# Performance work log

Measured on AMD Instinct MI355X. Metric: run time of the kernel, lower is better.

Reference implementation:

```python
import jax, jax.numpy as jnp
import numpy as np

N, E, G, T = 4096, 16384, 128, 100
DIMS = [(5, 64), (64, 128), (128, 256)]
EPS = 1e-5


def setup_inputs() -> dict:
    key = jax.random.key(0)
    ks = iter(jax.random.split(key, 64))
    d = {}
    d["x"] = jax.random.normal(next(ks), (N, 5), jnp.float32)
    d["edge_index"] = jax.random.randint(next(ks), (2, E), 0, N, jnp.int64)
    d["edge_attr"] = jax.random.uniform(next(ks), (E, 3), jnp.float32)
    d["batch_seg"] = jnp.sort(jax.random.randint(next(ks), (N,), 0, G, jnp.int64))
    for l, (cin, cout) in enumerate(DIMS, start=1):
        d[f"l{l}_W1"] = jax.random.normal(next(ks), (3, 32), jnp.float32) * 0.3
        d[f"l{l}_b1"] = jnp.zeros((32,), jnp.float32)
        d[f"l{l}_W2"] = jax.random.normal(next(ks), (32, cin * cout), jnp.float32) * 0.05
        d[f"l{l}_b2"] = jnp.zeros((cin * cout,), jnp.float32)
        d[f"l{l}_root"] = jax.random.normal(next(ks), (cin, cout), jnp.float32) * 0.1
        d[f"l{l}_bias"] = jnp.zeros((cout,), jnp.float32)
        d[f"bn{l}_g"] = jnp.ones((cout,), jnp.float32)
        d[f"bn{l}_b"] = jnp.zeros((cout,), jnp.float32)
        d[f"bn{l}_m"] = jax.random.normal(next(ks), (cout,), jnp.float32) * 0.01
        d[f"bn{l}_v"] = jax.random.uniform(next(ks), (cout,), jnp.float32, 0.5, 1.5)
    d["mlp_W"] = jax.random.normal(next(ks), (256, T), jnp.float32) * 0.06
    d["mlp_b"] = jnp.zeros((T,), jnp.float32)
    return d


def _nnconv(h, src, dst, edge_attr, W1, b1, W2, b2, root, bias, cin, cout):
    # edge MLP -> per-edge weight matrix [E, cin, cout]
    ew = (jax.nn.relu(edge_attr @ W1 + b1) @ W2 + b2).reshape(-1, cin, cout)
    msg = jnp.einsum('ei,eio->eo', h[src], ew)  # gather + per-edge matmul
    ssum = jax.ops.segment_sum(msg, dst, num_segments=N)
    cnt = jax.ops.segment_sum(jnp.ones((msg.shape[0],), msg.dtype), dst, num_segments=N)
    agg = ssum / jnp.maximum(cnt, 1.0)[:, None]  # scatter-mean
    return h @ root + agg + bias


def _bn(h, g, b, m, v):
    return g * (h - m) * jax.lax.rsqrt(v + EPS) + b


def reference(x, edge_index, edge_attr, batch_seg,
              l1_W1, l1_b1, l1_W2, l1_b2, l1_root, l1_bias, bn1_g, bn1_b, bn1_m, bn1_v,
              l2_W1, l2_b1, l2_W2, l2_b2, l2_root, l2_bias, bn2_g, bn2_b, bn2_m, bn2_v,
              l3_W1, l3_b1, l3_W2, l3_b2, l3_root, l3_bias, bn3_g, bn3_b, bn3_m, bn3_v,
              mlp_W, mlp_b):
    src, dst = edge_index[0], edge_index[1]
    h = _nnconv(x, src, dst, edge_attr, l1_W1, l1_b1, l1_W2, l1_b2, l1_root, l1_bias, 5, 64)
    h = jax.nn.relu(_bn(h, bn1_g, bn1_b, bn1_m, bn1_v))
    h = _nnconv(h, src, dst, edge_attr, l2_W1, l2_b1, l2_W2, l2_b2, l2_root, l2_bias, 64, 128)
    h = jax.nn.relu(_bn(h, bn2_g, bn2_b, bn2_m, bn2_v))
    h = _nnconv(h, src, dst, edge_attr, l3_W1, l3_b1, l3_W2, l3_b2, l3_root, l3_bias, 128, 256)
    h = jax.nn.relu(_bn(h, bn3_g, bn3_b, bn3_m, bn3_v))
    # global mean pool over graphs
    psum = jax.ops.segment_sum(h, batch_seg, num_segments=G)
    pcnt = jax.ops.segment_sum(jnp.ones((N,), h.dtype), batch_seg, num_segments=G)
    pooled = psum / jnp.maximum(pcnt, 1.0)[:, None]
    out = pooled @ mlp_W + mlp_b
    return jnp.where(out > 0, out, 0.1 * out)  # LeakyReLU(0.1)
```

## Files before the change

kernel.cpp:

```cpp
#include <hip/hip_runtime.h>
#include <cstdint>
#include <cstddef>

#define BN_EPS 1e-5f

typedef short bf16x8 __attribute__((ext_vector_type(8)));
typedef float f32x4  __attribute__((ext_vector_type(4)));
typedef unsigned short u16x8 __attribute__((ext_vector_type(8)));

__device__ __forceinline__ uint16_t f2bf_rte(float f) {
  uint32_t u = __float_as_uint(f);
  uint32_t r = u + 0x7fffu + ((u >> 16) & 1u);
  return (uint16_t)(r >> 16);
}
__device__ __forceinline__ float bf2f(uint16_t h) {
  return __uint_as_float(((uint32_t)h) << 16);
}
__device__ __forceinline__ void split_bf(float v, uint16_t& hi, uint16_t& lo) {
  hi = f2bf_rte(v);
  lo = f2bf_rte(v - bf2f(hi));
}

__device__ __forceinline__ void glds16(const uint16_t* g, uint16_t* l) {
  __builtin_amdgcn_global_load_lds(
      (const __attribute__((address_space(1))) uint32_t*)(const void*)g,
      (__attribute__((address_space(3))) uint32_t*)(void*)l, 16, 0, 0);
}

__global__ __launch_bounds__(1024) void csr_all_k(const int* __restrict__ dst,
                                                  int* __restrict__ offsets,
                                                  int* __restrict__ csr,
                                                  int N, int E) {
  __shared__ int cntS[4096];
  __shared__ int part[1024];
  const int t = threadIdx.x;
  for (int i = t; i < N; i += 1024) cntS[i] = 0;
  __syncthreads();
  for (int e = t; e < E; e += 1024) atomicAdd(&cntS[dst[e]], 1);
  __syncthreads();
  int a0 = cntS[4*t+0], a1 = cntS[4*t+1], a2 = cntS[4*t+2], a3 = cntS[4*t+3];
  part[t] = a0 + a1 + a2 + a3;
  __syncthreads();
  for (int off = 1; off < 1024; off <<= 1) {
    int v = (t >= off) ? part[t - off] : 0;
    __syncthreads();
    part[t] += v;
    __syncthreads();
  }
  int excl = (t == 0) ? 0 : part[t-1];
  int o0 = excl, o1 = o0 + a0, o2 = o1 + a1, o3 = o2 + a2;
  cntS[4*t+0] = o0; cntS[4*t+1] = o1; cntS[4*t+2] = o2; cntS[4*t+3] = o3;
  offsets[4*t+0] = o0; offsets[4*t+1] = o1; offsets[4*t+2] = o2; offsets[4*t+3] = o3;
  if (t == 0) offsets[N] = E;
  __syncthreads();
  for (int e = t; e < E; e += 1024) {
    int d = dst[e];
    int pos = atomicAdd(&cntS[d], 1);
    csr[pos] = e;
  }
}

__device__ __forceinline__ void w_elem(const float* __restrict__ W2, const float* __restrict__ b2,
                                       const float* __restrict__ root,
                                       uint16_t* __restrict__ Hi, uint16_t* __restrict__ Lo,
                                       int cin, int cout, int Kpad, int li) {
  int o  = li / Kpad;
  int ki = li - o * Kpad;
  float v = 0.f;
  if (ki < 34 * cin) {
    int k = ki / cin;
    int i = ki - k * cin;
    if (k < 32)       v = W2[(size_t)k * cin * cout + (size_t)i * cout + o];
    else if (k == 32) v = b2[(size_t)i * cout + o];
    else              v = root[(size_t)i * cout + o];
  }
  uint16_t hi, lo;
  split_bf(v, hi, lo);
  Hi[li] = hi;
  Lo[li] = lo;
}

__global__ void build_W3_k(const float* __restrict__ W2a, const float* __restrict__ b2a,
                           const float* __restrict__ roota, uint16_t* __restrict__ Hia,
                           uint16_t* __restrict__ Loa,
                           const float* __restrict__ W2b, const float* __restrict__ b2b,
                           const float* __restrict__ rootb, uint16_t* __restrict__ Hib,
                           uint16_t* __restrict__ Lob,
                           const float* __restrict__ W2c, const float* __restrict__ b2c,
                           const float* __restrict__ rootc, uint16_t* __restrict__ Hic,
                           uint16_t* __restrict__ Loc,
                           int e0, int e1, int e2) {
  int idx = blockIdx.x * blockDim.x + threadIdx.x;
  if (idx < e0)      w_elem(W2a, b2a, roota, Hia, Loa, 5,   64,  192,  idx);
  else if (idx < e1) w_elem(W2b, b2b, rootb, Hib, Lob, 64,  128, 2176, idx - e0);
  else if (idx < e2) w_elem(W2c, b2c, rootc, Hic, Loc, 128, 256, 4352, idx - e1);
}

template<int CIN>
__global__ __launch_bounds__(256) void build_S_vec_k(const float* __restrict__ h,
                                                     const float* __restrict__ ea,
                                                     const float* __restrict__ W1,
                                                     const float* __restrict__ b1,
                                                     const int* __restrict__ src,
                                                     const int* __restrict__ csr,
                                                     const int* __restrict__ offsets,
                                                     uint16_t* __restrict__ Shi,
                                                     uint16_t* __restrict__ Slo,
                                                     int Kpad) {
  constexpr int CH = 8;
  constexpr int K1 = 33 * CIN;
  constexpr int NCH = K1 / 8;
  constexpr int NP = (NCH + 255) / 256;
  __shared__ float hs[CH][CIN];
  __shared__ float zs[CH][33];
  __shared__ int   es[CH];
  const int n = blockIdx.x;
  const int tid = threadIdx.x;
  const int base = offsets[n];
  const int deg  = offsets[n+1] - base;
  const float scale = 1.f / fmaxf((float)deg, 1.f);
  float acc[NP][8];
#pragma unroll
  for (int p = 0; p < NP; p++)
#pragma unroll
    for (int j = 0; j < 8; j++) acc[p][j] = 0.f;

  for (int c0 = 0; c0 < deg; c0 += CH) {
    const int cc = min(CH, deg - c0);
    if (tid < cc) es[tid] = csr[base + c0 + tid];
    __syncthreads();
    for (int idx = tid; idx < cc * CIN; idx += 256) {
      int slot = idx / CIN, i = idx - slot * CIN;
      hs[slot][i] = h[(size_t)src[es[slot]] * CIN + i];
    }
    for (int idx = tid; idx < cc * 33; idx += 256) {
      int slot = idx / 33, k = idx - slot * 33;
      float v;
      if (k == 32) v = 1.f;
      else {
        int e = es[slot];
        v = fmaxf(ea[e*3+0] * W1[k] + ea[e*3+1] * W1[32 + k] + ea[e*3+2] * W1[64 + k] + b1[k], 0.f);
      }
      zs[slot][k] = v;
    }
    __syncthreads();
#pragma unroll
    for (int p = 0; p < NP; p++) {
      int ch = p * 256 + tid;
      if (ch < NCH) {
        int ki0 = ch * 8;
        int k  = ki0 / CIN;
        int i0 = ki0 & (CIN - 1);
        for (int c = 0; c < cc; c++) {
          float zv = zs[c][k];
          float4 h0 = *(const float4*)&hs[c][i0];
          float4 h1 = *(const float4*)&hs[c][i0 + 4];
          acc[p][0] += zv * h0.x; acc[p][1] += zv * h0.y;
          acc[p][2] += zv * h0.z; acc[p][3] += zv * h0.w;
          acc[p][4] += zv * h1.x; acc[p][5] += zv * h1.y;
          acc[p][6] += zv * h1.z; acc[p][7] += zv * h1.w;
        }
      }
    }
    __syncthreads();
  }
  const size_t rowb = (size_t)n * Kpad;
#pragma unroll
  for (int p = 0; p < NP; p++) {
    int ch = p * 256 + tid;
    if (ch < NCH) {
      u16x8 hv, lv;
#pragma unroll
      for (int j = 0; j < 8; j++) {
        uint16_t hi, lo;
        split_bf(acc[p][j] * scale, hi, lo);
        hv[j] = hi; lv[j] = lo;
      }
      *(u16x8*)(Shi + rowb + ch * 8) = hv;
      *(u16x8*)(Slo + rowb + ch * 8) = lv;
    }
  }
  for (int c = tid; c < CIN / 8; c += 256) {
    int i0 = c * 8;
    float4 a = *(const float4*)&h[(size_t)n * CIN + i0];
    float4 b = *(const float4*)&h[(size_t)n * CIN + i0 + 4];
    float vals[8] = {a.x, a.y, a.z, a.w, b.x, b.y, b.z, b.w};
    u16x8 hv, lv;
#pragma unroll
    for (int j = 0; j < 8; j++) {
      uint16_t hi, lo;
      split_bf(vals[j], hi, lo);
      hv[j] = hi; lv[j] = lo;
    }
    *(u16x8*)(Shi + rowb + K1 + i0) = hv;
    *(u16x8*)(Slo + rowb + K1 + i0) = lv;
  }
  for (int ki = 34 * CIN + tid; ki < Kpad; ki += 256) {
    Shi[rowb + ki] = 0;
    Slo[rowb + ki] = 0;
  }
}

__global__ __launch_bounds__(256) void build_S5_k(const float* __restrict__ h,
                                                  const float* __restrict__ ea,
                                                  const float* __restrict__ W1,
                                                  const float* __restrict__ b1,
                                                  const int* __restrict__ src,
                                                  const int* __restrict__ csr,
                                                  const int* __restrict__ offsets,
                                                  uint16_t* __restrict__ Shi,
                                                  uint16_t* __restrict__ Slo,
                                                  int Kpad) {
  constexpr int CIN = 5, CH = 8;
  constexpr int K1 = 33 * CIN;
  constexpr int KT = 34 * CIN;
  __shared__ float hs[CH][CIN];
  __shared__ float zs[CH][33];
  __shared__ int   es[CH];
  const int n = blockIdx.x;
  const int tid = threadIdx.x;
  const int base = offsets[n];
  const int deg  = offsets[n+1] - base;
  const float scale = 1.f / fmaxf((float)deg, 1.f);
  float acc = 0.f;

  for (int c0 = 0; c0 < deg; c0 += CH) {
    const int cc = min(CH, deg - c0);
    if (tid < cc) es[tid] = csr[base + c0 + tid];
    __syncthreads();
    for (int idx = tid; idx < cc * CIN; idx += 256) {
      int slot = idx / CIN, i = idx - slot * CIN;
      hs[slot][i] = h[(size_t)src[es[slot]] * CIN + i];
    }
    for (int idx = tid; idx < cc * 33; idx += 256) {
      int slot = idx / 33, k = idx - slot * 33;
      float v;
      if (k == 32) v = 1.f;
      else {
        int e = es[slot];
        v = fmaxf(ea[e*3+0] * W1[k] + ea[e*3+1] * W1[32 + k] + ea[e*3+2] * W1[64 + k] + b1[k], 0.f);
      }
      zs[slot][k] = v;
    }
    __syncthreads();
    if (tid < K1) {
      int k = tid / CIN, i = tid - (tid / CIN) * CIN;
      float a = acc;
      for (int c = 0; c < cc; c++) a += zs[c][k] * hs[c][i];
      acc = a;
    }
    __syncthreads();
  }
  const size_t rowb = (size_t)n * Kpad;
  if (tid < K1) {
    uint16_t hi, lo;
    split_bf(acc * scale, hi, lo);
    Shi[rowb + tid] = hi;
    Slo[rowb + tid] = lo;
  }
  if (tid < CIN) {
    uint16_t hi, lo;
    split_bf(h[(size_t)n * CIN + tid], hi, lo);
    Shi[rowb + K1 + tid] = hi;
    Slo[rowb + K1 + tid] = lo;
  }
  for (int ki = KT + tid; ki < Kpad; ki += 256) {
    Shi[rowb + ki] = 0;
    Slo[rowb + ki] = 0;
  }
}

template<int BN, int KS>
__global__ __launch_bounds__(256, 1) void mfma_gemm2_k(const uint16_t* __restrict__ Ahi,
                                                       const uint16_t* __restrict__ Alo,
                                                       const uint16_t* __restrict__ Bhi,
                                                       const uint16_t* __restrict__ Blo,
                                                       float* __restrict__ Cpart,
                                                       int Kpad, int Ncol, int M,
                                                       int totalIters) {
  constexpr int BM = 128;
  constexpr int FN = BN / 32;
  constexpr int SLOTS = KS / 8;
  constexpr int RPC = 2048 / KS;
  constexpr int NCA = BM / RPC;
  constexpr int NCB = BN / RPC;
  constexpr int OAH = 0;
  constexpr int OAL = BM * KS;
  constexpr int OBH = 2 * BM * KS;
  constexpr int OBL = 2 * BM * KS + BN * KS;
  constexpr int BUFSZ = (2 * BM + 2 * BN) * KS;
  __shared__ uint16_t smem[2 * BUFSZ] __attribute__((aligned(16)));

  const int z  = blockIdx.x;
  const int m0 = blockIdx.y * BM;
  const int n0 = blockIdx.z * BN;
  const int SK = gridDim.x;
  const int itBeg = (int)((long long)totalIters * z / SK);
  const int itEnd = (int)((long long)totalIters * (z + 1) / SK);
  const int nsteps = itEnd - itBeg;

  const int tid  = threadIdx.x;
  const int lane = tid & 63;
  const int wave = tid >> 6;
  const int wm = wave & 1, wn = wave >> 1;
  const int q  = lane >> 4;
  const int mr = lane & 15;

  const int srow  = tid / SLOTS;
  const int sslot = tid & (SLOTS - 1);
  const int sx    = (KS == 64) ? (srow & 7) : ((srow >> 1) & 3);
  const int swz   = (sslot ^ sx) * 8;
  size_t aoff[NCA], boff[NCB];
#pragma unroll
  for (int c = 0; c < NCA; c++)
    aoff[c] = (size_t)(m0 + c * RPC + srow) * Kpad + swz + (size_t)itBeg * KS;
#pragma unroll
  for (int c = 0; c < NCB; c++)
    boff[c] = (size_t)(n0 + c * RPC + srow) * Kpad + swz + (size_t)itBeg * KS;
  const int wlds = wave << 9;

  f32x4 acc[4][FN];
#pragma unroll
  for (int a = 0; a < 4; a++)
#pragma unroll
    for (int b = 0; b < FN; b++) acc[a][b] = (f32x4)0.f;

  auto stage = [&](int buf, int t) {
    uint16_t* base = smem + buf * BUFSZ;
    const size_t ka = (size_t)t * KS;
#pragma unroll
    for (int c = 0; c < NCA; c++) {
      glds16(Ahi + aoff[c] + ka, base + OAH + c * 2048 + wlds);
      glds16(Alo + aoff[c] + ka, base + OAL + c * 2048 + wlds);
    }
#pragma unroll
    for (int c = 0; c < NCB; c++) {
      glds16(Bhi + boff[c] + ka, base + OBH + c * 2048 + wlds);
      glds16(Blo + boff[c] + ka, base + OBL + c * 2048 + wlds);
    }
  };

  const int xr = (KS == 64) ? (mr & 7) : ((mr >> 1) & 3);

  if (nsteps > 0) stage(0, 0);
  for (int t = 0; t < nsteps; t++) {
    __syncthreads();
    if (t + 1 < nsteps) stage((t & 1) ^ 1, t + 1);
    const uint16_t* B_ = smem + (t & 1) * BUFSZ;
#pragma unroll
    for (int ks = 0; ks < KS / 32; ks++) {
      const int e0 = (ks * 32 + q * 8) ^ (xr << 3);
      bf16x8 ah[4], al[4], bh[FN], bl[FN];
#pragma unroll
      for (int f = 0; f < 4; f++) {
        const int row = wm * 64 + f * 16 + mr;
        ah[f] = *(const bf16x8*)&B_[OAH + row * KS + e0];
        al[f] = *(const bf16x8*)&B_[OAL + row * KS + e0];
      }
#pragma unroll
      for (int f = 0; f < FN; f++) {
        const int row = wn * (BN / 2) + f * 16 + mr;
        bh[f] = *(const bf16x8*)&B_[OBH + row * KS + e0];
        bl[f] = *(const bf16x8*)&B_[OBL + row * KS + e0];
      }
#pragma unroll
      for (int fm = 0; fm < 4; fm++)
#pragma unroll
        for (int fn = 0; fn < FN; fn++) {
          acc[fm][fn] = __builtin_amdgcn_mfma_f32_16x16x32_bf16(ah[fm], bh[fn], acc[fm][fn], 0, 0, 0);
          acc[fm][fn] = __builtin_amdgcn_mfma_f32_16x16x32_bf16(ah[fm], bl[fn], acc[fm][fn], 0, 0, 0);
          acc[fm][fn] = __builtin_amdgcn_mfma_f32_16x16x32_bf16(al[fm], bh[fn], acc[fm][fn], 0, 0, 0);
        }
    }
  }

  float* Cz = Cpart + (size_t)z * M * Ncol;
#pragma unroll
  for (int fm = 0; fm < 4; fm++) {
#pragma unroll
    for (int reg = 0; reg < 4; reg++) {
      const int row = m0 + wm * 64 + fm * 16 + q * 4 + reg;
#pragma unroll
      for (int fn = 0; fn < FN; fn++) {
        const int col = n0 + wn * (BN / 2) + fn * 16 + mr;
        Cz[(size_t)row * Ncol + col] = acc[fm][fn][reg];
      }
    }
  }
}

__global__ void epilogue_k(const float* __restrict__ Cpart, int SK, size_t plane4,
                           int Ncol,
                           const float* __restrict__ bias, const float* __restrict__ bg,
                           const float* __restrict__ bb, const float* __restrict__ bnm,
                           const float* __restrict__ bnv,
                           float* __restrict__ C, int total4) {
  int i = blockIdx.x * blockDim.x + threadIdx.x;
  if (i >= total4) return;
  float4 v = {0.f, 0.f, 0.f, 0.f};
  for (int z = 0; z < SK; z++) {
    float4 p = *((const float4*)Cpart + (size_t)z * plane4 + i);
    v.x += p.x; v.y += p.y; v.z += p.z; v.w += p.w;
  }
  int col0 = (i * 4) % Ncol;
  float o[4] = {v.x, v.y, v.z, v.w};
#pragma unroll
  for (int j = 0; j < 4; j++) {
    int c = col0 + j;
    float s = bg[c] * rsqrtf(bnv[c] + BN_EPS);
    float val = (o[j] + bias[c] - bnm[c]) * s + bb[c];
    o[j] = fmaxf(val, 0.f);
  }
  float4 r = {o[0], o[1], o[2], o[3]};
  *((float4*)C + i) = r;
}

__global__ __launch_bounds__(256) void pool_final_k(const float* __restrict__ h,
                                                    const int* __restrict__ seg,
                                                    const float* __restrict__ W,
                                                    const float* __restrict__ b,
                                                    float* __restrict__ out,
                                                    int N, int T) {
  __shared__ float pooled[256];
  const int g = blockIdx.x, tid = threadIdx.x;
  int lo = 0, hi = N;
  while (lo < hi) { int mid = (lo + hi) >> 1; if (seg[mid] < g) lo = mid + 1; else hi = mid; }
  int lo2 = lo, hi2 = N;
  while (lo2 < hi2) { int mid = (lo2 + hi2) >> 1; if (seg[mid] < g + 1) lo2 = mid + 1; else hi2 = mid; }
  const int cnt = lo2 - lo;
  const float inv = 1.f / fmaxf((float)cnt, 1.f);
  float s = 0.f;
  for (int n = lo; n < lo2; n++) s += h[(size_t)n * 256 + tid];
  pooled[tid] = s * inv;
  __syncthreads();
  if (tid < T) {
    float acc = b[tid];
    for (int o = 0; o < 256; o++) acc += pooled[o] * W[(size_t)o * T + tid];
    out[(size_t)g * T + tid] = (acc > 0.f) ? acc : 0.1f * acc;
  }
}

extern "C" void kernel_launch(void* const* d_in, const int* in_sizes, int n_in,
                              void* d_out, int out_size, void* d_ws, size_t ws_size,
                              hipStream_t stream) {
  const float* x   = (const float*)d_in[0];
  const int*   ei  = (const int*)d_in[1];
  const float* ea  = (const float*)d_in[2];
  const int*   seg = (const int*)d_in[3];

  const int N = in_sizes[0] / 5;
  const int E = in_sizes[2] / 3;
  const int T = in_sizes[35];
  const int G = out_size / T;
  const int* src = ei;
  const int* dst = ei + E;

  const float *W1[3], *b1[3], *W2[3], *b2[3], *root[3], *bias[3];
  const float *bng[3], *bnb[3], *bnm[3], *bnv[3];
  for (int l = 0; l < 3; l++) {
    int base = 4 + l * 10;
    W1[l]   = (const float*)d_in[base + 0];
    b1[l]   = (const float*)d_in[base + 1];
    W2[l]   = (const float*)d_in[base + 2];
    b2[l]   = (const float*)d_in[base + 3];
    root[l] = (const float*)d_in[base + 4];
    bias[l] = (const float*)d_in[base + 5];
    bng[l]  = (const float*)d_in[base + 6];
    bnb[l]  = (const float*)d_in[base + 7];
    bnm[l]  = (const float*)d_in[base + 8];
    bnv[l]  = (const float*)d_in[base + 9];
  }
  const float* mlpW = (const float*)d_in[34];
  const float* mlpb = (const float*)d_in[35];

  char* p = (char*)d_ws;
  auto carve = [&](size_t bytes) -> char* {
    char* r = p;
    p += (bytes + 255) & ~(size_t)255;
    return r;
  };
  const int KPADMAX = 4352;
  const int cins[3]   = {5, 64, 128};
  const int couts[3]  = {64, 128, 256};
  const int kpads[3]  = {192, 2176, 4352};
  const int sks[3]    = {3, 8, 8};
  const int ksteps[3] = {64, 64, 32};

  int*      offsets = (int*)carve((size_t)(N + 1) * 4);
  int*      csr     = (int*)carve((size_t)E * 4);
  uint16_t* WhiL[3]; uint16_t* WloL[3];
  for (int l = 0; l < 3; l++) {
    WhiL[l] = (uint16_t*)carve((size_t)couts[l] * kpads[l] * 2);
    WloL[l] = (uint16_t*)carve((size_t)couts[l] * kpads[l] * 2);
  }
  uint16_t* Shi     = (uint16_t*)carve((size_t)N * KPADMAX * 2);
  uint16_t* Slo     = (uint16_t*)carve((size_t)N * KPADMAX * 2);
  float*    Cpart   = (float*)carve((size_t)8 * N * 256 * 4);
  float*    hA      = (float*)carve((size_t)N * 256 * 4);
  float*    hB      = (float*)carve((size_t)N * 128 * 4);

  csr_all_k<<<1, 1024, 0, stream>>>(dst, offsets, csr, N, E);

  {
    int t0 = couts[0] * kpads[0];
    int t1 = couts[1] * kpads[1];
    int t2 = couts[2] * kpads[2];
    int e0 = t0, e1 = t0 + t1, e2 = t0 + t1 + t2;
    build_W3_k<<<(e2 + 255) / 256, 256, 0, stream>>>(
        W2[0], b2[0], root[0], WhiL[0], WloL[0],
        W2[1], b2[1], root[1], WhiL[1], WloL[1],
        W2[2], b2[2], root[2], WhiL[2], WloL[2],
        e0, e1, e2);
  }

  const float* hin = x;
  float* houts[3] = {hA, hB, hA};

  for (int l = 0; l < 3; l++) {
    int cin = cins[l], cout = couts[l], Kpad = kpads[l], SK = sks[l];
    int iters = Kpad / ksteps[l];
    if (cin == 5)
      build_S5_k<<<N, 256, 0, stream>>>(hin, ea, W1[l], b1[l], src, csr, offsets, Shi, Slo, Kpad);
    else if (cin == 64)
      build_S_vec_k<64><<<N, 256, 0, stream>>>(hin, ea, W1[l], b1[l], src, csr, offsets, Shi, Slo, Kpad);
    else
      build_S_vec_k<128><<<N, 256, 0, stream>>>(hin, ea, W1[l], b1[l], src, csr, offsets, Shi, Slo, Kpad);

    if (cout == 256) {
      dim3 grid(SK, N / 128, 1);
      mfma_gemm2_k<256, 32><<<grid, 256, 0, stream>>>(Shi, Slo, WhiL[l], WloL[l], Cpart,
                                                      Kpad, cout, N, iters);
    } else if (cout == 128) {
      dim3 grid(SK, N / 128, 1);
      mfma_gemm2_k<128, 64><<<grid, 256, 0, stream>>>(Shi, Slo, WhiL[l], WloL[l], Cpart,
                                                      Kpad, cout, N, iters);
    } else {
      dim3 grid(SK, N / 128, 1);
      mfma_gemm2_k<64, 64><<<grid, 256, 0, stream>>>(Shi, Slo, WhiL[l], WloL[l], Cpart,
                                                     Kpad, cout, N, iters);
    }

    int total4 = N * cout / 4;
    epilogue_k<<<(total4 + 255) / 256, 256, 0, stream>>>(Cpart, SK, (size_t)N * cout / 4, cout,
                                                         bias[l], bng[l], bnb[l], bnm[l], bnv[l],
                                                         houts[l], total4);
    hin = houts[l];
  }

  pool_final_k<<<G, 256, 0, stream>>>(hA, seg, mlpW, mlpb, (float*)d_out, N, T);
}
```

Measured before the change: 283.5 us.

## Raise GEMM occupancy with single-buffered wide tile and uniform split-K of sixteen

Replaces the split-K MFMA GEMM with a variant that allows two blocks per CU and uses a K step of 32 for every layer. For the cout=256 layer it drops LDS double buffering and reorders the inner loop to load B fragments per column, which cuts LDS and register use so more blocks fit per CU. Split-K rises to 16 for all layers, giving more parallelism but larger partial buffers for the epilogue to reduce. The single-buffered path gives up overlap of global-to-LDS loads with MFMA work within a block and adds a second barrier per step.

```diff
diff --git a/kernel.cpp b/kernel.cpp
--- a/kernel.cpp
+++ b/kernel.cpp
@@ -270,8 +270,8 @@
   }
 }
 
-template<int BN, int KS>
-__global__ __launch_bounds__(256, 1) void mfma_gemm2_k(const uint16_t* __restrict__ Ahi,
+template<int BN, int KS, bool DBUF>
+__global__ __launch_bounds__(256, 2) void mfma_gemm3_k(const uint16_t* __restrict__ Ahi,
                                                        const uint16_t* __restrict__ Alo,
                                                        const uint16_t* __restrict__ Bhi,
                                                        const uint16_t* __restrict__ Blo,
@@ -289,7 +289,8 @@
   constexpr int OBH = 2 * BM * KS;
   constexpr int OBL = 2 * BM * KS + BN * KS;
   constexpr int BUFSZ = (2 * BM + 2 * BN) * KS;
-  __shared__ uint16_t smem[2 * BUFSZ] __attribute__((aligned(16)));
+  constexpr int NB = DBUF ? 2 : 1;
+  __shared__ uint16_t smem[NB * BUFSZ] __attribute__((aligned(16)));
 
   const int z  = blockIdx.x;
   const int m0 = blockIdx.y * BM;
@@ -342,35 +343,67 @@
 
   const int xr = (KS == 64) ? (mr & 7) : ((mr >> 1) & 3);
 
-  if (nsteps > 0) stage(0, 0);
-  for (int t = 0; t < nsteps; t++) {
-    __syncthreads();
-    if (t + 1 < nsteps) stage((t & 1) ^ 1, t + 1);
-    const uint16_t* B_ = smem + (t & 1) * BUFSZ;
-#pragma unroll
-    for (int ks = 0; ks < KS / 32; ks++) {
-      const int e0 = (ks * 32 + q * 8) ^ (xr << 3);
-      bf16x8 ah[4], al[4], bh[FN], bl[FN];
-#pragma unroll
-      for (int f = 0; f < 4; f++) {
-        const int row = wm * 64 + f * 16 + mr;
-        ah[f] = *(const bf16x8*)&B_[OAH + row * KS + e0];
-        al[f] = *(const bf16x8*)&B_[OAL + row * KS + e0];
-      }
-#pragma unroll
-      for (int f = 0; f < FN; f++) {
-        const int row = wn * (BN / 2) + f * 16 + mr;
-        bh[f] = *(const bf16x8*)&B_[OBH + row * KS + e0];
-        bl[f] = *(const bf16x8*)&B_[OBL + row * KS + e0];
-      }
-#pragma unroll
-      for (int fm = 0; fm < 4; fm++)
+  if (DBUF) {
+    if (nsteps > 0) stage(0, 0);
+    for (int t = 0; t < nsteps; t++) {
+      __syncthreads();
+      if (t + 1 < nsteps) stage((t & 1) ^ 1, t + 1);
+      const uint16_t* B_ = smem + (t & 1) * BUFSZ;
+#pragma unroll
+      for (int ks = 0; ks < KS / 32; ks++) {
+        const int e0 = (ks * 32 + q * 8) ^ (xr << 3);
+        bf16x8 ah[4], al[4], bh[FN], bl[FN];
+#pragma unroll
+        for (int f = 0; f < 4; f++) {
+          const int row = wm * 64 + f * 16 + mr;
+          ah[f] = *(const bf16x8*)&B_[OAH + row * KS + e0];
+          al[f] = *(const bf16x8*)&B_[OAL + row * KS + e0];
+        }
+#pragma unroll
+        for (int f = 0; f < FN; f++) {
+          const int row = wn * (BN / 2) + f * 16 + mr;
+          bh[f] = *(const bf16x8*)&B_[OBH + row * KS + e0];
+          bl[f] = *(const bf16x8*)&B_[OBL + row * KS + e0];
+        }
+#pragma unroll
+        for (int fm = 0; fm < 4; fm++)
+#pragma unroll
+          for (int fn = 0; fn < FN; fn++) {
+            acc[fm][fn] = __builtin_amdgcn_mfma_f32_16x16x32_bf16(ah[fm], bh[fn], acc[fm][fn], 0, 0, 0);
+            acc[fm][fn] = __builtin_amdgcn_mfma_f32_16x16x32_bf16(ah[fm], bl[fn], acc[fm][fn], 0, 0, 0);
+            acc[fm][fn] = __builtin_amdgcn_mfma_f32_16x16x32_bf16(al[fm], bh[fn], acc[fm][fn], 0, 0, 0);
+          }
+      }
+    }
+  } else {
+    for (int t = 0; t < nsteps; t++) {
+      stage(0, t);
+      __syncthreads();
+      const uint16_t* B_ = smem;
+#pragma unroll
+      for (int ks = 0; ks < KS / 32; ks++) {
+        const int e0 = (ks * 32 + q * 8) ^ (xr << 3);
+        bf16x8 ah[4], al[4];
+#pragma unroll
+        for (int f = 0; f < 4; f++) {
+          const int row = wm * 64 + f * 16 + mr;
+          ah[f] = *(const bf16x8*)&B_[OAH + row * KS + e0];
+          al[f] = *(const bf16x8*)&B_[OAL + row * KS + e0];
+        }
 #pragma unroll
         for (int fn = 0; fn < FN; fn++) {
-          acc[fm][fn] = __builtin_amdgcn_mfma_f32_16x16x32_bf16(ah[fm], bh[fn], acc[fm][fn], 0, 0, 0);
-          acc[fm][fn] = __builtin_amdgcn_mfma_f32_16x16x32_bf16(ah[fm], bl[fn], acc[fm][fn], 0, 0, 0);
-          acc[fm][fn] = __builtin_amdgcn_mfma_f32_16x16x32_bf16(al[fm], bh[fn], acc[fm][fn], 0, 0, 0);
+          const int row = wn * (BN / 2) + fn * 16 + mr;
+          bf16x8 bhv = *(const bf16x8*)&B_[OBH + row * KS + e0];
+          bf16x8 blv = *(const bf16x8*)&B_[OBL + row * KS + e0];
+#pragma unroll
+          for (int fm = 0; fm < 4; fm++) {
+            acc[fm][fn] = __builtin_amdgcn_mfma_f32_16x16x32_bf16(ah[fm], bhv, acc[fm][fn], 0, 0, 0);
+            acc[fm][fn] = __builtin_amdgcn_mfma_f32_16x16x32_bf16(ah[fm], blv, acc[fm][fn], 0, 0, 0);
+            acc[fm][fn] = __builtin_amdgcn_mfma_f32_16x16x32_bf16(al[fm], bhv, acc[fm][fn], 0, 0, 0);
+          }
         }
+      }
+      __syncthreads();
     }
   }
 
@@ -483,8 +516,7 @@
   const int cins[3]   = {5, 64, 128};
   const int couts[3]  = {64, 128, 256};
   const int kpads[3]  = {192, 2176, 4352};
-  const int sks[3]    = {3, 8, 8};
-  const int ksteps[3] = {64, 64, 32};
+  const int SK = 16;
 
   int*      offsets = (int*)carve((size_t)(N + 1) * 4);
   int*      csr     = (int*)carve((size_t)E * 4);
@@ -495,7 +527,7 @@
   }
   uint16_t* Shi     = (uint16_t*)carve((size_t)N * KPADMAX * 2);
   uint16_t* Slo     = (uint16_t*)carve((size_t)N * KPADMAX * 2);
-  float*    Cpart   = (float*)carve((size_t)8 * N * 256 * 4);
+  float*    Cpart   = (float*)carve((size_t)SK * N * 256 * 4);
   float*    hA      = (float*)carve((size_t)N * 256 * 4);
   float*    hB      = (float*)carve((size_t)N * 128 * 4);
 
@@ -517,8 +549,8 @@
   float* houts[3] = {hA, hB, hA};
 
   for (int l = 0; l < 3; l++) {
-    int cin = cins[l], cout = couts[l], Kpad = kpads[l], SK = sks[l];
-    int iters = Kpad / ksteps[l];
+    int cin = cins[l], cout = couts[l], Kpad = kpads[l];
+    int iters = Kpad / 32;
     if (cin == 5)
       build_S5_k<<<N, 256, 0, stream>>>(hin, ea, W1[l], b1[l], src, csr, offsets, Shi, Slo, Kpad);
     else if (cin == 64)
@@ -526,19 +558,16 @@
     else
       build_S_vec_k<128><<<N, 256, 0, stream>>>(hin, ea, W1[l], b1[l], src, csr, offsets, Shi, Slo, Kpad);
 
-    if (cout == 256) {
-      dim3 grid(SK, N / 128, 1);
-      mfma_gemm2_k<256, 32><<<grid, 256, 0, stream>>>(Shi, Slo, WhiL[l], WloL[l], Cpart,
-                                                      Kpad, cout, N, iters);
-    } else if (cout == 128) {
-      dim3 grid(SK, N / 128, 1);
-      mfma_gemm2_k<128, 64><<<grid, 256, 0, stream>>>(Shi, Slo, WhiL[l], WloL[l], Cpart,
-                                                      Kpad, cout, N, iters);
-    } else {
-      dim3 grid(SK, N / 128, 1);
-      mfma_gemm2_k<64, 64><<<grid, 256, 0, stream>>>(Shi, Slo, WhiL[l], WloL[l], Cpart,
-                                                     Kpad, cout, N, iters);
-    }
+    dim3 grid(SK, N / 128, 1);
+    if (cout == 256)
+      mfma_gemm3_k<256, 32, false><<<grid, 256, 0, stream>>>(Shi, Slo, WhiL[l], WloL[l], Cpart,
+                                                             Kpad, cout, N, iters);
+    else if (cout == 128)
+      mfma_gemm3_k<128, 32, true><<<grid, 256, 0, stream>>>(Shi, Slo, WhiL[l], WloL[l], Cpart,
+                                                            Kpad, cout, N, iters);
+    else
+      mfma_gemm3_k<64, 32, true><<<grid, 256, 0, stream>>>(Shi, Slo, WhiL[l], WloL[l], Cpart,
+                                                           Kpad, cout, N, iters);
 
     int total4 = N * cout / 4;
     epilogue_k<<<(total4 + 255) / 256, 256, 0, stream>>>(Cpart, SK, (size_t)N * cout / 4, cout,
```

Result: slower. 300.3 us (+5.9%).
